# Kernel optimization log

Measured on AMD Instinct MI355X. Metric: run time of the kernel, lower is better.

## Reference

```python
import jax, jax.numpy as jnp
import numpy as np
import math

B, S, D, H = 2, 2048, 1024, 16
DK = D // H

def setup_inputs() -> dict:
    key = jax.random.key(0)
    ks = jax.random.split(key, 8)
    query = jax.random.normal(ks[0], (B, S, D), dtype=jnp.float32)
    k_in = jax.random.normal(ks[1], (B, S, D), dtype=jnp.float32)
    value = jax.random.normal(ks[2], (B, S, D), dtype=jnp.float32)
    mask = jax.random.randint(ks[3], (B, S, S), 0, 2, dtype=jnp.int32)
    scale = 1.0 / math.sqrt(D)
    Wq = jax.random.normal(ks[4], (D, D), dtype=jnp.float32) * scale
    Wk = jax.random.normal(ks[5], (D, D), dtype=jnp.float32) * scale
    Wv = jax.random.normal(ks[6], (D, D), dtype=jnp.float32) * scale
    Wo = jax.random.normal(ks[7], (D, D), dtype=jnp.float32) * scale
    return {"query": query, "key": k_in, "value": value, "mask": mask,
            "Wq": Wq, "Wk": Wk, "Wv": Wv, "Wo": Wo}

def reference(query, key, value, mask, Wq, Wk, Wv, Wo):
    # torch Linear(no bias): y = x @ W.T ; weights are [out, in]
    def split_heads(x):  # [B,S,D] -> [B,H,S,DK]
        return x.reshape(B, S, H, DK).transpose(0, 2, 1, 3)
    q = split_heads(query @ Wq.T)
    k = split_heads(key @ Wk.T)
    v = split_heads(value @ Wv.T)
    scores = jnp.einsum('bhqd,bhkd->bhqk', q, k) / jnp.sqrt(jnp.float32(DK))
    scores = jnp.where(mask[:, None, :, :] == 0, jnp.float32(-1e9), scores)
    p_attn = jax.nn.softmax(scores, axis=-1)  # dropout is identity in eval mode
    attn = jnp.einsum('bhqk,bhkd->bhqd', p_attn, v)
    out = attn.transpose(0, 2, 1, 3).reshape(B, S, D)
    return out @ Wo.T
```

## Files before the change

### kernel.cpp

```cpp
#include <hip/hip_runtime.h>
#include <hip/hip_bf16.h>
#include <cstdint>
#include <cstddef>

constexpr int BATCH = 2;
constexpr int SEQ   = 2048;
constexpr int DIM   = 1024;
constexpr int NH    = 16;
constexpr int DK    = 64;

typedef unsigned short u16;
typedef unsigned int   u32;
typedef unsigned long long u64;

typedef __attribute__((ext_vector_type(8))) short bf16x8;
typedef __attribute__((ext_vector_type(8))) unsigned short u16x8;
typedef __attribute__((ext_vector_type(4))) float f32x4;
typedef __attribute__((ext_vector_type(16))) float f32x16;
typedef __attribute__((ext_vector_type(4))) unsigned int u32x4;

__device__ __forceinline__ u16 f2bf(float f) {
  u32 u = __builtin_bit_cast(u32, f);
  u32 r = (u + 0x7FFFu + ((u >> 16) & 1u)) >> 16;
  return (u16)r;
}

__device__ __forceinline__ u32 pack_bf2(float a, float b) {
  __hip_bfloat162 h2 = __float22bfloat162_rn(make_float2(a, b));
  u32 r;
  __builtin_memcpy(&r, &h2, 4);
  return r;
}

__device__ __forceinline__ float fexp2(float x) {
#if __has_builtin(__builtin_amdgcn_exp2f)
  return __builtin_amdgcn_exp2f(x);
#else
  return exp2f(x);
#endif
}

__device__ __forceinline__ void plswap32(u32& a, u32& b) {
  asm volatile("v_permlane32_swap_b32 %0, %1" : "+v"(a), "+v"(b));
}

__device__ __forceinline__ void gload16(const u16* g, u16* l) {
  __builtin_amdgcn_global_load_lds(
      (const __attribute__((address_space(1))) void*)g,
      (__attribute__((address_space(3))) void*)l, 16, 0, 0);
}

constexpr size_t QS  = (size_t)BATCH * SEQ * DIM;
constexpr size_t WSZ = (size_t)DIM * DIM;
constexpr int CVT_BLOCKS  = (int)((3 * QS + 4 * WSZ) / (256 * 8));
constexpr int MASK_BLOCKS = (BATCH * SEQ * SEQ) / 256;

__global__ __launch_bounds__(256) void prep(const float* __restrict__ q,
                                            const float* __restrict__ k,
                                            const float* __restrict__ v,
                                            const float* __restrict__ wq,
                                            const float* __restrict__ wk,
                                            const float* __restrict__ wv,
                                            const float* __restrict__ wo,
                                            u16* __restrict__ dst,
                                            const int* __restrict__ mask,
                                            u64* __restrict__ bits) {
  const int bid = blockIdx.x;
  if (bid < CVT_BLOCKS) {
    const size_t i = ((size_t)bid * 256 + threadIdx.x) * 8;
    const float* s;
    if      (i < QS)              s = q  + i;
    else if (i < 2 * QS)          s = k  + (i - QS);
    else if (i < 3 * QS)          s = v  + (i - 2 * QS);
    else if (i < 3 * QS + WSZ)     s = wq + (i - 3 * QS);
    else if (i < 3 * QS + 2 * WSZ) s = wk + (i - 3 * QS - WSZ);
    else if (i < 3 * QS + 3 * WSZ) s = wv + (i - 3 * QS - 2 * WSZ);
    else                           s = wo + (i - 3 * QS - 3 * WSZ);
    f32x4 a = *(const f32x4*)s, b2 = *(const f32x4*)(s + 4);
    u32x4 t;
    t[0] = pack_bf2(a[0], a[1]);  t[1] = pack_bf2(a[2], a[3]);
    t[2] = pack_bf2(b2[0], b2[1]); t[3] = pack_bf2(b2[2], b2[3]);
    *(u16x8*)(dst + i) = __builtin_bit_cast(u16x8, t);
  } else {
    const int gt = (bid - CVT_BLOCKS) * 256 + threadIdx.x;
    u64 m = __ballot(mask[gt] != 0);
    if ((threadIdx.x & 63) == 0) bits[gt >> 6] = m;
  }
}

__global__ __launch_bounds__(256) void transpose_v(const u16* __restrict__ V,
                                                   u16* __restrict__ Vt) {
  __shared__ u16 t[64][68];
  const int st = blockIdx.x * 64;
  const int bh = blockIdx.y;
  const int b = bh >> 4, h = bh & 15;
  const int tid = threadIdx.x;
#pragma unroll
  for (int s = 0; s < 2; ++s) {
    int c = tid + s * 256;
    int row = c >> 3, c8 = c & 7;
    u16x8 vv = *(const u16x8*)(V + ((size_t)(b * SEQ + st + row)) * DIM + h * DK + c8 * 8);
#pragma unroll
    for (int j = 0; j < 8; ++j) t[row][c8 * 8 + j] = vv[j];
  }
  __syncthreads();
#pragma unroll
  for (int s = 0; s < 2; ++s) {
    int c = tid + s * 256;
    int dk = c >> 3, sc = c & 7;
    u16x8 ov;
#pragma unroll
    for (int j = 0; j < 8; ++j) ov[j] = t[sc * 8 + j][dk];
    *(u16x8*)(Vt + ((size_t)bh * DK + dk) * SEQ + st + sc * 8) = ov;
  }
}

struct GemmParams {
  const void* A[3];
  const void* B[3];
  void*       C[3];
  float       alpha[3];
};

template <bool OUTF32>
__global__ __launch_bounds__(256) void gemm_nt(GemmParams p, int M, int N, int K) {
  const int z = blockIdx.z;
  __shared__ __align__(16) u16 As[128 * 32];
  __shared__ __align__(16) u16 Bs[128 * 32];

  const int tid = threadIdx.x;
  const int lane = tid & 63, w = tid >> 6;
  const int l31 = lane & 31, hi = lane >> 5;
  const int bm = blockIdx.y * 128, bn = blockIdx.x * 128;
  const int wm = (w >> 1) * 64, wn = (w & 1) * 64;

  const u16* A = (const u16*)p.A[z];
  const u16* B = (const u16*)p.B[z];

  const int sr0 = w * 32 + (lane >> 2);
  const int scol = (lane & 3) * 8;
  u16* const lA0 = &As[(w * 32) * 32];
  u16* const lA1 = &As[(w * 32 + 16) * 32];
  u16* const lB0 = &Bs[(w * 32) * 32];
  u16* const lB1 = &Bs[(w * 32 + 16) * 32];

  f32x16 acc[2][2] = {};

  for (int k0 = 0; k0 < K; k0 += 32) {
    gload16(&A[(size_t)(bm + sr0) * K + k0 + scol],      lA0);
    gload16(&A[(size_t)(bm + sr0 + 16) * K + k0 + scol], lA1);
    gload16(&B[(size_t)(bn + sr0) * K + k0 + scol],      lB0);
    gload16(&B[(size_t)(bn + sr0 + 16) * K + k0 + scol], lB1);
    __syncthreads();

#pragma unroll
    for (int ks = 0; ks < 2; ++ks) {
      bf16x8 af[2], bf[2];
#pragma unroll
      for (int mb = 0; mb < 2; ++mb)
        af[mb] = *(const bf16x8*)&As[(wm + mb * 32 + l31) * 32 + ks * 16 + hi * 8];
#pragma unroll
      for (int nb = 0; nb < 2; ++nb)
        bf[nb] = *(const bf16x8*)&Bs[(wn + nb * 32 + l31) * 32 + ks * 16 + hi * 8];
#pragma unroll
      for (int mb = 0; mb < 2; ++mb)
#pragma unroll
        for (int nb = 0; nb < 2; ++nb)
          acc[mb][nb] = __builtin_amdgcn_mfma_f32_32x32x16_bf16(af[mb], bf[nb], acc[mb][nb], 0, 0, 0);
    }
    __syncthreads();
  }

  const float alpha = p.alpha[z];
#pragma unroll
  for (int mb = 0; mb < 2; ++mb)
#pragma unroll
    for (int nb = 0; nb < 2; ++nb)
#pragma unroll
      for (int r = 0; r < 16; ++r) {
        const int row = bm + wm + mb * 32 + (r & 3) + 8 * (r >> 2) + 4 * hi;
        const int col = bn + wn + nb * 32 + l31;
        float val = acc[mb][nb][r] * alpha;
        if (OUTF32) ((float*)p.C[z])[(size_t)row * N + col] = val;
        else        ((u16*)p.C[z])[(size_t)row * N + col]  = f2bf(val);
      }
}

__global__ __launch_bounds__(512, 2) void attn_fwd(const u16* __restrict__ Qb,
                                                   const u16* __restrict__ Kb,
                                                   const u16* __restrict__ Vtb,
                                                   const u64* __restrict__ mbits,
                                                   u16* __restrict__ Ob) {
  const int h = blockIdx.y, b = blockIdx.z;
  const int tid = threadIdx.x;
  const int lane = tid & 63, w = tid >> 6;
  const int l31 = lane & 31, hi = lane >> 5;
  const int half = w >> 2, wq = w & 3;

  __shared__ __align__(16) u16 SB[2 * 16384];
  __shared__ float Lsh[4][64];

  const int q0 = blockIdx.x * 128 + wq * 32;
  const int rsw = l31 & 7;

  bf16x8 qreg[4];
  {
    const u16* qp = Qb + ((size_t)(b * SEQ + q0 + l31)) * DIM + h * DK + 8 * hi;
#pragma unroll
    for (int s = 0; s < 4; ++s) qreg[s] = *(const bf16x8*)(qp + 16 * s);
  }

  const int grow = (w << 3) + (lane >> 3);
  const int gchk = (lane & 7) ^ (grow & 7);
  const u16* kbase  = Kb + ((size_t)b * SEQ + grow) * DIM + h * DK + gchk * 8;
  const u16* vtbase = Vtb + ((size_t)(b * NH + h) * DK + grow) * SEQ + gchk * 8;
  const u64* mrow   = mbits + (size_t)(b * SEQ + q0 + l31) * (SEQ / 64) + half * 16;

  f32x16 o[2] = {};
  float lsum = 0.f;

  {
    u16* const nb = SB;
    gload16(kbase,                          nb + 0     + w * 512);
    gload16(kbase + (size_t)1024 * DIM,     nb + 4096  + w * 512);
    gload16(vtbase,                         nb + 8192  + w * 512);
    gload16(vtbase + 1024,                  nb + 12288 + w * 512);
  }
  u64 mbc = mrow[0];
  __syncthreads();

  for (int kt = 0; kt < 16; ++kt) {
    const int cur = kt & 1;
    u64 mbn = mbc;
    if (kt < 15) {
      u16* const nb = SB + (cur ^ 1) * 16384;
      const u16* ks = kbase + (size_t)(kt + 1) * 64 * DIM;
      const u16* vs = vtbase + (kt + 1) * 64;
      gload16(ks,                       nb + 0     + w * 512);
      gload16(ks + (size_t)1024 * DIM,  nb + 4096  + w * 512);
      gload16(vs,                       nb + 8192  + w * 512);
      gload16(vs + 1024,                nb + 12288 + w * 512);
      mbn = mrow[kt + 1];
    }
    const u16* const Kc = SB + cur * 16384 + half * 4096;
    const u16* const Vc = SB + cur * 16384 + 8192 + half * 4096;

    const u64 nmb = ~mbc;
    const u64 mbh = nmb >> (hi * 4);
    const u32 nm[2] = {(u32)mbh, (u32)(mbh >> 32)};
    f32x16 sc[2];
#pragma unroll
    for (int kb = 0; kb < 2; ++kb)
#pragma unroll
      for (int r = 0; r < 16; ++r) {
        const int key = (r & 3) + 8 * (r >> 2);
        u32 t = (u32)(((int)(nm[kb] << (31 - key))) >> 31) & 0xC6EA6000u;
        sc[kb][r] = __builtin_bit_cast(float, t);
      }

#pragma unroll
    for (int kb = 0; kb < 2; ++kb) {
      const int row = kb * 32 + l31;
#pragma unroll
      for (int s = 0; s < 4; ++s) {
        bf16x8 kf = *(const bf16x8*)&Kc[row * 64 + ((2 * s + hi) ^ rsw) * 8];
        sc[kb] = __builtin_amdgcn_mfma_f32_32x32x16_bf16(kf, qreg[s], sc[kb], 0, 0, 0);
      }
    }

#pragma unroll
    for (int kb = 0; kb < 2; ++kb)
#pragma unroll
      for (int r = 0; r < 16; ++r)
        sc[kb][r] = fexp2(sc[kb][r]);
    float s8[8];
#pragma unroll
    for (int i = 0; i < 8; ++i)
      s8[i] = (sc[0][i] + sc[0][i + 8]) + (sc[1][i] + sc[1][i + 8]);
    lsum += ((s8[0] + s8[1]) + (s8[2] + s8[3])) + ((s8[4] + s8[5]) + (s8[6] + s8[7]));

#pragma unroll
    for (int kb = 0; kb < 2; ++kb) {
      u32 wv[8];
#pragma unroll
      for (int t = 0; t < 8; ++t)
        wv[t] = pack_bf2(sc[kb][2 * t], sc[kb][2 * t + 1]);
      plswap32(wv[0], wv[2]);
      plswap32(wv[1], wv[3]);
      plswap32(wv[4], wv[6]);
      plswap32(wv[5], wv[7]);
      u32x4 f0 = {wv[0], wv[1], wv[2], wv[3]};
      u32x4 f1 = {wv[4], wv[5], wv[6], wv[7]};
      bf16x8 pa0 = __builtin_bit_cast(bf16x8, f0);
      bf16x8 pa1 = __builtin_bit_cast(bf16x8, f1);
#pragma unroll
      for (int ks = 0; ks < 2; ++ks) {
        bf16x8 pf = ks ? pa1 : pa0;
#pragma unroll
        for (int d = 0; d < 2; ++d) {
          const int row = l31 + 32 * d;
          bf16x8 vf = *(const bf16x8*)&Vc[row * 64 + ((4 * kb + 2 * ks + hi) ^ rsw) * 8];
          o[d] = __builtin_amdgcn_mfma_f32_32x32x16_bf16(pf, vf, o[d], 0, 0, 0);
        }
      }
    }
    mbc = mbn;
    __syncthreads();
  }

  lsum += __shfl_xor(lsum, 32, 64);
  f32x4* const oa4 = (f32x4*)SB;
  if (half == 1) {
    f32x4* dst = oa4 + (size_t)(wq * 64 + lane) * 8;
#pragma unroll
    for (int d = 0; d < 2; ++d)
#pragma unroll
      for (int cc = 0; cc < 4; ++cc) {
        f32x4 t = {o[d][cc * 4 + 0], o[d][cc * 4 + 1], o[d][cc * 4 + 2], o[d][cc * 4 + 3]};
        dst[(d * 4 + cc) ^ (lane & 7)] = t;
      }
    Lsh[wq][lane] = lsum;
  }
  __syncthreads();
  if (half == 0) {
    const float ltot = lsum + Lsh[wq][lane];
    const float linv = 1.0f / ltot;
    const f32x4* src = oa4 + (size_t)(wq * 64 + lane) * 8;
    f32x4 ov[8];
#pragma unroll
    for (int c = 0; c < 8; ++c) ov[c] = src[c ^ (lane & 7)];
    float lr[16];
#pragma unroll
    for (int r = 0; r < 16; ++r)
      lr[r] = __shfl(linv, (r & 3) + 8 * (r >> 2) + 4 * hi, 64);
#pragma unroll
    for (int d = 0; d < 2; ++d)
#pragma unroll
      for (int r = 0; r < 16; ++r) {
        const float om = o[d][r] + ov[d * 4 + (r >> 2)][r & 3];
        const int qloc = (r & 3) + 8 * (r >> 2) + 4 * hi;
        Ob[(size_t)(b * SEQ + q0 + qloc) * DIM + h * DK + l31 + 32 * d] = f2bf(om * lr[r]);
      }
  }
}

extern "C" void kernel_launch(void* const* d_in, const int* in_sizes, int n_in,
                              void* d_out, int out_size, void* d_ws, size_t ws_size,
                              hipStream_t stream) {
  const float* q    = (const float*)d_in[0];
  const float* k    = (const float*)d_in[1];
  const float* v    = (const float*)d_in[2];
  const int*   mask = (const int*)d_in[3];
  const float* Wq   = (const float*)d_in[4];
  const float* Wk   = (const float*)d_in[5];
  const float* Wv   = (const float*)d_in[6];
  const float* Wo   = (const float*)d_in[7];
  float* out = (float*)d_out;

  char* ws = (char*)d_ws;
  u64* mbits = (u64*)ws;
  u16* XB  = (u16*)(ws + 0x0100000);
  u16* xq = XB, *xk = XB + QS, *xv = XB + 2 * QS;
  u16* wqb = XB + 3 * QS, *wkb = wqb + WSZ, *wvb = wkb + WSZ, *wob = wvb + WSZ;
  u16* Qb  = (u16*)(ws + 0x2100000);
  u16* Kb  = (u16*)(ws + 0x2900000);
  u16* Vb  = (u16*)(ws + 0x3100000);
  u16* Vtb = (u16*)(ws + 0x3900000);
  u16* Ab  = (u16*)(ws + 0x4100000);

  prep<<<CVT_BLOCKS + MASK_BLOCKS, 256, 0, stream>>>(q, k, v, Wq, Wk, Wv, Wo, XB,
                                                     mask, mbits);

  GemmParams gp;
  gp.A[0] = xq;  gp.A[1] = xk;  gp.A[2] = xv;
  gp.B[0] = wqb; gp.B[1] = wkb; gp.B[2] = wvb;
  gp.C[0] = Qb;  gp.C[1] = Kb;  gp.C[2] = Vb;
  gp.alpha[0] = 0.125f * 1.44269504088896f; gp.alpha[1] = 1.0f; gp.alpha[2] = 1.0f;
  gemm_nt<false><<<dim3(DIM / 128, (BATCH * SEQ) / 128, 3), 256, 0, stream>>>(
      gp, BATCH * SEQ, DIM, DIM);

  transpose_v<<<dim3(SEQ / 64, BATCH * NH), 256, 0, stream>>>(Vb, Vtb);

  attn_fwd<<<dim3(SEQ / 128, NH, BATCH), 512, 0, stream>>>(Qb, Kb, Vtb, mbits, Ab);

  GemmParams go;
  go.A[0] = Ab; go.B[0] = wob; go.C[0] = out; go.alpha[0] = 1.0f;
  go.A[1] = go.A[2] = nullptr; go.B[1] = go.B[2] = nullptr; go.C[1] = go.C[2] = nullptr;
  go.alpha[1] = go.alpha[2] = 1.0f;
  gemm_nt<true><<<dim3(DIM / 128, (BATCH * SEQ) / 128, 1), 256, 0, stream>>>(
      go, BATCH * SEQ, DIM, DIM);
}
```

Measured before the change: 155.1 us.

## Load K/V fragments directly from global memory, dropping LDS double buffering

The attention kernel no longer stages K and V tiles through double-buffered shared memory with per-iteration barriers. Each wave now loads its MFMA operand fragments straight from global memory into registers. This removes LDS traffic and the __syncthreads in the loop. The cost is redundant global/L2 reads, since the four query waves in a block each fetch the same K/V, and load latency is now exposed without software prefetch.

```diff
diff --git a/kernel.cpp b/kernel.cpp
--- a/kernel.cpp
+++ b/kernel.cpp
@@ -197,11 +197,10 @@
   const int l31 = lane & 31, hi = lane >> 5;
   const int half = w >> 2, wq = w & 3;
 
-  __shared__ __align__(16) u16 SB[2 * 16384];
+  __shared__ __align__(16) f32x4 oa4[2048];
   __shared__ float Lsh[4][64];
 
   const int q0 = blockIdx.x * 128 + wq * 32;
-  const int rsw = l31 & 7;
 
   bf16x8 qreg[4];
   {
@@ -210,40 +209,24 @@
     for (int s = 0; s < 4; ++s) qreg[s] = *(const bf16x8*)(qp + 16 * s);
   }
 
-  const int grow = (w << 3) + (lane >> 3);
-  const int gchk = (lane & 7) ^ (grow & 7);
-  const u16* kbase  = Kb + ((size_t)b * SEQ + grow) * DIM + h * DK + gchk * 8;
-  const u16* vtbase = Vtb + ((size_t)(b * NH + h) * DK + grow) * SEQ + gchk * 8;
-  const u64* mrow   = mbits + (size_t)(b * SEQ + q0 + l31) * (SEQ / 64) + half * 16;
+  const u16* pK0 = Kb + ((size_t)b * SEQ + half * 1024 + l31) * DIM + h * DK + hi * 8;
+  const u16* pK1 = pK0 + (size_t)32 * DIM;
+  const u16* pV0 = Vtb + ((size_t)(b * NH + h) * DK + l31) * SEQ + half * 1024 + hi * 8;
+  const u16* pV1 = pV0 + (size_t)32 * SEQ;
+  const u64* mrow = mbits + (size_t)(b * SEQ + q0 + l31) * (SEQ / 64) + half * 16;
 
   f32x16 o[2] = {};
   float lsum = 0.f;
-
-  {
-    u16* const nb = SB;
-    gload16(kbase,                          nb + 0     + w * 512);
-    gload16(kbase + (size_t)1024 * DIM,     nb + 4096  + w * 512);
-    gload16(vtbase,                         nb + 8192  + w * 512);
-    gload16(vtbase + 1024,                  nb + 12288 + w * 512);
-  }
   u64 mbc = mrow[0];
-  __syncthreads();
 
   for (int kt = 0; kt < 16; ++kt) {
-    const int cur = kt & 1;
-    u64 mbn = mbc;
-    if (kt < 15) {
-      u16* const nb = SB + (cur ^ 1) * 16384;
-      const u16* ks = kbase + (size_t)(kt + 1) * 64 * DIM;
-      const u16* vs = vtbase + (kt + 1) * 64;
-      gload16(ks,                       nb + 0     + w * 512);
-      gload16(ks + (size_t)1024 * DIM,  nb + 4096  + w * 512);
-      gload16(vs,                       nb + 8192  + w * 512);
-      gload16(vs + 1024,                nb + 12288 + w * 512);
-      mbn = mrow[kt + 1];
-    }
-    const u16* const Kc = SB + cur * 16384 + half * 4096;
-    const u16* const Vc = SB + cur * 16384 + 8192 + half * 4096;
+    bf16x8 ka[4], kb2[4];
+#pragma unroll
+    for (int s = 0; s < 4; ++s) {
+      ka[s]  = *(const bf16x8*)(pK0 + s * 16);
+      kb2[s] = *(const bf16x8*)(pK1 + s * 16);
+    }
+    const u64 mbn = (kt < 15) ? mrow[kt + 1] : 0ull;
 
     const u64 nmb = ~mbc;
     const u64 mbh = nmb >> (hi * 4);
@@ -259,13 +242,16 @@
       }
 
 #pragma unroll
-    for (int kb = 0; kb < 2; ++kb) {
-      const int row = kb * 32 + l31;
-#pragma unroll
-      for (int s = 0; s < 4; ++s) {
-        bf16x8 kf = *(const bf16x8*)&Kc[row * 64 + ((2 * s + hi) ^ rsw) * 8];
-        sc[kb] = __builtin_amdgcn_mfma_f32_32x32x16_bf16(kf, qreg[s], sc[kb], 0, 0, 0);
-      }
+    for (int s = 0; s < 4; ++s) {
+      sc[0] = __builtin_amdgcn_mfma_f32_32x32x16_bf16(ka[s],  qreg[s], sc[0], 0, 0, 0);
+      sc[1] = __builtin_amdgcn_mfma_f32_32x32x16_bf16(kb2[s], qreg[s], sc[1], 0, 0, 0);
+    }
+
+    bf16x8 va[4], vb[4];
+#pragma unroll
+    for (int c = 0; c < 4; ++c) {
+      va[c] = *(const bf16x8*)(pV0 + c * 16);
+      vb[c] = *(const bf16x8*)(pV1 + c * 16);
     }
 
 #pragma unroll
@@ -296,20 +282,19 @@
 #pragma unroll
       for (int ks = 0; ks < 2; ++ks) {
         bf16x8 pf = ks ? pa1 : pa0;
-#pragma unroll
-        for (int d = 0; d < 2; ++d) {
-          const int row = l31 + 32 * d;
-          bf16x8 vf = *(const bf16x8*)&Vc[row * 64 + ((4 * kb + 2 * ks + hi) ^ rsw) * 8];
-          o[d] = __builtin_amdgcn_mfma_f32_32x32x16_bf16(pf, vf, o[d], 0, 0, 0);
-        }
+        const int c = 2 * kb + ks;
+        o[0] = __builtin_amdgcn_mfma_f32_32x32x16_bf16(pf, va[c], o[0], 0, 0, 0);
+        o[1] = __builtin_amdgcn_mfma_f32_32x32x16_bf16(pf, vb[c], o[1], 0, 0, 0);
       }
     }
     mbc = mbn;
-    __syncthreads();
+    pK0 += (size_t)64 * DIM;
+    pK1 += (size_t)64 * DIM;
+    pV0 += 64;
+    pV1 += 64;
   }
 
   lsum += __shfl_xor(lsum, 32, 64);
-  f32x4* const oa4 = (f32x4*)SB;
   if (half == 1) {
     f32x4* dst = oa4 + (size_t)(wq * 64 + lane) * 8;
 #pragma unroll
```

New measurement: 229.8 us. 48.2% more time.
